# Kernel optimization log

Hardware: AMD Instinct MI355X
Metric: run time of the kernel (lower is better)

## Reference

```python
import jax, jax.numpy as jnp
import numpy as np

TOP_K = 2
NUM_EXPERTS = 64
TEMPERATURE = 1.0

def setup_inputs() -> dict:
    key = jax.random.key(0)
    ks = jax.random.split(key, 4)
    B, L, D, DT, E = 4, 4096, 2048, 16, NUM_EXPERTS
    return {
        "x": jax.random.normal(ks[0], (B, L, D), dtype=jnp.float32),
        "z_task": jax.random.normal(ks[1], (B, DT), dtype=jnp.float32),
        "W_router": jax.random.normal(ks[2], (E, D + DT), dtype=jnp.float32) * 0.02,
        "W_task_proj": jax.random.normal(ks[3], (DT, DT), dtype=jnp.float32) * 0.25,
        "b_task_proj": jnp.zeros((DT,), dtype=jnp.float32),
        "expert_bias": jnp.zeros((E,), dtype=jnp.float32),
    }

def reference(x, z_task, W_router, W_task_proj, b_task_proj, expert_bias):
    B, L, D = x.shape
    E = W_router.shape[0]
    DT = z_task.shape[-1]
    # task_proj: Linear(d_task, d_task) + exact GELU
    tp = jax.nn.gelu(z_task @ W_task_proj.T + b_task_proj, approximate=False)  # [B, DT]
    # concat fusion: logits = [x ; task_proj] @ W_router^T, split to avoid materializing concat
    logits = (jnp.einsum('bld,ed->ble', x, W_router[:, :D])
              + jnp.einsum('bt,et->be', tp, W_router[:, D:])[:, None, :]
              + expert_bias)  # [B, L, E]
    probs = jax.nn.softmax(logits / TEMPERATURE, axis=-1)
    topw, topi = jax.lax.top_k(probs, TOP_K)  # [B, L, K]
    topw = topw / (topw.sum(axis=-1, keepdims=True) + 1e-8)
    # aux load-balance loss: E * sum_i f_i * P_i over flattened tokens
    mask = jax.nn.one_hot(topi, E, dtype=probs.dtype).sum(axis=-2) / TOP_K  # [B, L, E]
    f = mask.reshape(-1, E).mean(axis=0)
    P = probs.reshape(-1, E).mean(axis=0)
    aux_loss = E * (f * P).sum()
    return topw, topi, probs, aux_loss
```

## Files before the change

kernel.cpp:

```cpp
#include <hip/hip_runtime.h>
#include <math.h>


#define DDIM 2048
#define WROW 2064

typedef unsigned int u32;
typedef unsigned short u16;
typedef unsigned long long u64;
using short8 = __attribute__((ext_vector_type(8))) short;
using f32x4  = __attribute__((ext_vector_type(4))) float;

typedef const __attribute__((address_space(1))) u32* gp1;
typedef __attribute__((address_space(3))) u32* lp3;

#define BAR() do {                                                              \
        __builtin_amdgcn_s_barrier();                                           \
        asm volatile("" ::: "memory");                                          \
        __builtin_amdgcn_sched_barrier(0);                                      \
    } while (0)

__device__ __forceinline__ u16 bf16rne(float f) {
    u32 u = __float_as_uint(f);
    return (u16)((u + 0x7FFFu + ((u >> 16) & 1u)) >> 16);
}

__global__ void k0_wsplit(const float* __restrict__ Wr, u32* __restrict__ wh,
                          u32* __restrict__ wl) {
    const int g = blockIdx.x * 256 + threadIdx.x;
    const int e  = g >> 10;
    const int kp = g & 1023;
    const int k  = kp * 2;
    const int step = k >> 5, kb = (k >> 3) & 3, d = (k >> 1) & 3;
    const int grp = e >> 4, lane = kb * 16 + (e & 15);
    const float w0 = Wr[(size_t)e * WROW + k];
    const float w1 = Wr[(size_t)e * WROW + k + 1];
    const u16 h0 = bf16rne(w0);
    const u16 h1 = bf16rne(w1);
    const u16 l0 = bf16rne(w0 - __uint_as_float((u32)h0 << 16));
    const u16 l1 = bf16rne(w1 - __uint_as_float((u32)h1 << 16));
    const u32 oi = (u32)(((step * 4 + grp) * 64 + lane) * 4 + d);
    wh[oi] = ((u32)h1 << 16) | h0;
    wl[oi] = ((u32)l1 << 16) | l0;
}

__global__ void k1_task(const float* __restrict__ z, const float* __restrict__ Wp,
                        const float* __restrict__ bp, const float* __restrict__ Wr,
                        const float* __restrict__ eb, float* __restrict__ wsb) {
    __shared__ float tp[4][16];
    const int t = threadIdx.x;
    if (t < 64) {
        const int b = t >> 4, r = t & 15;
        float s = bp[r];
        #pragma unroll
        for (int i = 0; i < 16; ++i) s += z[b * 16 + i] * Wp[r * 16 + i];
        tp[b][r] = 0.5f * s * (1.0f + erff(s * 0.70710678118654752440f));
    }
    #pragma unroll
    for (int i = t; i < 1024; i += 256) wsb[256 + i] = 0.0f;
    __syncthreads();
    {
        const int b = t >> 6, e = t & 63;
        const float* wr = Wr + (size_t)e * WROW + DDIM;
        float s = eb[e];
        #pragma unroll
        for (int i = 0; i < 16; ++i) s += tp[b][i] * wr[i];
        wsb[b * 64 + e] = s;
    }
}

__global__ __launch_bounds__(576, 1) void k2_mfma(const float* __restrict__ x,
                                                  const float* __restrict__ wsb,
                                                  const u32* __restrict__ whp,
                                                  const u32* __restrict__ wlp,
                                                  float* __restrict__ wacc,
                                                  float* __restrict__ out) {
    __shared__ __align__(16) u32  bbuf[2][4096];
    __shared__ float lg[2][64 * 68];
    __shared__ float pf[8 * 128];

    const int tid   = threadIdx.x;
    const int wv    = __builtin_amdgcn_readfirstlane(tid >> 6);
    const int lane  = tid & 63;
    const int tok0b = blockIdx.x * 64;
    const int bb    = tok0b >> 12;

    if (wv == 8) {
#define BDMA(t, buf) do {                                                       \
            _Pragma("unroll")                                                   \
            for (int hl = 0; hl < 2; ++hl)                                      \
            _Pragma("unroll")                                                   \
            for (int hh = 0; hh < 2; ++hh)                                      \
            _Pragma("unroll")                                                   \
            for (int g = 0; g < 4; ++g) {                                       \
                const u32* _s = (hl ? wlp : whp) +                              \
                                ((t) + hh * 32) * 1024 + g * 256 + lane * 4;    \
                u32* _d = &bbuf[buf][hl * 2048 + hh * 1024 + g * 256 + lane * 4];\
                __builtin_amdgcn_global_load_lds((gp1)_s, (lp3)_d, 16, 0, 0);   \
            }                                                                   \
        } while (0)
        BDMA(0, 0);
        asm volatile("s_waitcnt vmcnt(0)" ::: "memory");
        BAR();
        for (int t = 0; t < 32; ++t) {
            if (t < 31) {
                BDMA(t + 1, (t + 1) & 1);
                asm volatile("s_waitcnt vmcnt(0)" ::: "memory");
            }
            BAR();
        }
#undef BDMA
    } else {
        const int tg  = wv & 3;
        const int h   = wv >> 2;
        const int row = lane & 15;
        const int kg  = lane >> 4;
        const int tok0 = tok0b + tg * 16;

        f32x4 acc[4];
        #pragma unroll
        for (int g = 0; g < 4; ++g) {
            const float tl = (h == 0) ? wsb[bb * 64 + g * 16 + row] : 0.0f;
            acc[g] = (f32x4){tl, tl, tl, tl};
        }
        #pragma unroll
        for (int g = 0; g < 4; ++g) asm volatile("" : "+v"(acc[g]));
        __builtin_amdgcn_sched_barrier(0);

        const u64 xaddr = (u64)(x + (size_t)(tok0 + row) * DDIM + h * 1024 + kg * 8);
        f32x4 xr[6][2];

#define XLOAD(i, T) do {                                                        \
            asm volatile("global_load_dwordx4 %0, %1, off offset:%c2"           \
                : "=&v"(xr[i][0]) : "v"(xaddr), "i"((T) * 128));                \
            asm volatile("global_load_dwordx4 %0, %1, off offset:%c2"           \
                : "=&v"(xr[i][1]) : "v"(xaddr), "i"((T) * 128 + 16));           \
        } while (0)

#define XWAIT(i) do {                                                           \
            asm volatile("s_waitcnt vmcnt(10)"                                  \
                : "+v"(xr[i][0]), "+v"(xr[i][1]));                              \
            __builtin_amdgcn_sched_barrier(0);                                  \
        } while (0)

#define MSTEP(xa, xb, BH, BL) do {                                              \
            float vv[8];                                                        \
            _Pragma("unroll")                                                   \
            for (int j = 0; j < 4; ++j) { vv[j] = (xa)[j]; vv[4 + j] = (xb)[j]; }\
            short8 Ah, Al;                                                      \
            _Pragma("unroll")                                                   \
            for (int j = 0; j < 8; ++j) {                                       \
                const float v = vv[j];                                          \
                const u16 hh = bf16rne(v);                                      \
                const u16 ll = bf16rne(v - __uint_as_float((u32)hh << 16));     \
                Ah[j] = (short)hh; Al[j] = (short)ll;                           \
            }                                                                   \
            _Pragma("unroll")                                                   \
            for (int g = 0; g < 4; ++g) {                                       \
                acc[g] = __builtin_amdgcn_mfma_f32_16x16x32_bf16(Ah, BH[g], acc[g], 0, 0, 0); \
                acc[g] = __builtin_amdgcn_mfma_f32_16x16x32_bf16(Ah, BL[g], acc[g], 0, 0, 0); \
                acc[g] = __builtin_amdgcn_mfma_f32_16x16x32_bf16(Al, BH[g], acc[g], 0, 0, 0); \
                acc[g] = __builtin_amdgcn_mfma_f32_16x16x32_bf16(Al, BL[g], acc[g], 0, 0, 0); \
            }                                                                   \
        } while (0)

        XLOAD(0, 0); XLOAD(1, 1); XLOAD(2, 2);
        XLOAD(3, 3); XLOAD(4, 4); XLOAD(5, 5);
        BAR();
        #pragma unroll
        for (int t = 0; t < 32; ++t) {
            short8 BH[4], BL[4];
            #pragma unroll
            for (int g = 0; g < 4; ++g) {
                BH[g] = *(const short8*)&bbuf[t & 1][h * 1024 + g * 256 + lane * 4];
                BL[g] = *(const short8*)&bbuf[t & 1][2048 + h * 1024 + g * 256 + lane * 4];
            }
            XWAIT(t % 6);
            MSTEP(xr[t % 6][0], xr[t % 6][1], BH, BL);
            XLOAD(t % 6, (t + 6) & 31);
            BAR();
        }
        asm volatile("s_waitcnt vmcnt(0)"
            : "+v"(xr[0][0]), "+v"(xr[0][1]), "+v"(xr[1][0]), "+v"(xr[1][1]),
              "+v"(xr[2][0]), "+v"(xr[2][1]), "+v"(xr[3][0]), "+v"(xr[3][1]),
              "+v"(xr[4][0]), "+v"(xr[4][1]), "+v"(xr[5][0]), "+v"(xr[5][1]));
        __builtin_amdgcn_sched_barrier(0);
#undef XLOAD
#undef XWAIT
#undef MSTEP

        #pragma unroll
        for (int g = 0; g < 4; ++g)
            #pragma unroll
            for (int r = 0; r < 4; ++r)
                lg[h][(tg * 16 + kg * 4 + r) * 68 + g * 16 + row] = acc[g][r];
    }

    __syncthreads();

    if (wv < 8) {
        float pacc = 0.0f, facc = 0.0f;
        for (int i = 0; i < 8; ++i) {
            const int tk = wv * 8 + i;
            const float v = lg[0][tk * 68 + lane] + lg[1][tk * 68 + lane];
            float m1 = v; int i1 = lane;
            #pragma unroll
            for (int off = 32; off; off >>= 1) {
                const float ov = __shfl_xor(m1, off, 64);
                const int   oi = __shfl_xor(i1, off, 64);
                if (ov > m1 || (ov == m1 && oi < i1)) { m1 = ov; i1 = oi; }
            }
            const float vx = (lane == i1) ? -3.4e38f : v;
            float m2 = vx; int i2 = lane;
            #pragma unroll
            for (int off = 32; off; off >>= 1) {
                const float ov = __shfl_xor(m2, off, 64);
                const int   oi = __shfl_xor(i2, off, 64);
                if (ov > m2 || (ov == m2 && oi < i2)) { m2 = ov; i2 = oi; }
            }
            const float p = __expf(v - m1);
            float s = p;
            #pragma unroll
            for (int off = 32; off; off >>= 1) s += __shfl_xor(s, off, 64);
            const float rZ = 1.0f / s;
            const float pn = p * rZ;
            const int   T  = tok0b + tk;
            out[65536 + (size_t)T * 64 + lane] = pn;
            pacc += pn;
            facc += (lane == i1 ? 1.0f : 0.0f) + (lane == i2 ? 1.0f : 0.0f);
            if (lane == 0) {
                const float q1 = rZ, q2 = __expf(m2 - m1) * rZ;
                const float dn = 1.0f / (q1 + q2 + 1e-8f);
                float2 tw; tw.x = q1 * dn; tw.y = q2 * dn;
                *(float2*)(out + (size_t)T * 2) = tw;
                float2 ti; ti.x = (float)i1; ti.y = (float)i2;
                *(float2*)(out + 32768 + (size_t)T * 2) = ti;
            }
        }
        pf[wv * 128 + lane]      = pacc;
        pf[wv * 128 + 64 + lane] = facc;
    }
    __syncthreads();

    if (wv == 0) {
        float ps = 0.0f, fs = 0.0f;
        #pragma unroll
        for (int w2 = 0; w2 < 8; ++w2) {
            ps += pf[w2 * 128 + lane];
            fs += pf[w2 * 128 + 64 + lane];
        }
        const int slot = blockIdx.x & 7;
        atomicAdd(wacc + slot * 128 + lane, ps);
        atomicAdd(wacc + slot * 128 + 64 + lane, fs);
    }
}

__global__ void k3_aux(const float* __restrict__ wsb, float* __restrict__ out) {
    const int e = threadIdx.x;
    float P = 0.0f, F = 0.0f;
    #pragma unroll
    for (int s = 0; s < 8; ++s) {
        P += wsb[256 + s * 128 + e];
        F += wsb[256 + s * 128 + 64 + e];
    }
    float val = P * F;
    #pragma unroll
    for (int off = 32; off; off >>= 1) val += __shfl_xor(val, off, 64);
    if (e == 0)
        out[1114112] = 64.0f * val / (16384.0f * 2.0f * 16384.0f);
}

extern "C" void kernel_launch(void* const* d_in, const int* in_sizes, int n_in,
                              void* d_out, int out_size, void* d_ws, size_t ws_size,
                              hipStream_t stream) {
    (void)in_sizes; (void)n_in; (void)out_size; (void)ws_size;
    const float* x  = (const float*)d_in[0];
    const float* z  = (const float*)d_in[1];
    const float* Wr = (const float*)d_in[2];
    const float* Wp = (const float*)d_in[3];
    const float* bp = (const float*)d_in[4];
    const float* eb = (const float*)d_in[5];
    float* out = (float*)d_out;
    float* wsb = (float*)d_ws;
    u32*   wfH = (u32*)(wsb + 1280);
    u32*   wfL = wfH + 65536;

    hipLaunchKernelGGL(k0_wsplit, dim3(256), dim3(256), 0, stream, Wr, wfH, wfL);
    hipLaunchKernelGGL(k1_task,   dim3(1),   dim3(256), 0, stream, z, Wp, bp, Wr, eb, wsb);
    hipLaunchKernelGGL(k2_mfma,   dim3(256), dim3(576), 0, stream, x, wsb,
                       wfH, wfL, wsb + 256, out);
    hipLaunchKernelGGL(k3_aux,    dim3(1),   dim3(64),  0, stream, wsb, out);
}
```

Baseline: 55.90 us.

## Triple-buffer router weight DMA and alias LDS buffers into one pool

The producer wave now keeps two weight tiles in flight through a three-slot LDS ring, using a partial vmcnt wait instead of draining all loads before each barrier. The double-buffer, logits and partial-sum arrays are merged into one aliased shared pool so the extra slot adds no LDS. This is meant to hide global-to-LDS load latency behind the MFMA loop. Aliasing the logit scratch over the weight buffers depends on every DMA being finished before the epilogue writes to them, and the ring adds a modulo-3 index.

```diff
diff --git a/kernel.cpp b/kernel.cpp
--- a/kernel.cpp
+++ b/kernel.cpp
@@ -75,9 +75,9 @@
                                                   const u32* __restrict__ wlp,
                                                   float* __restrict__ wacc,
                                                   float* __restrict__ out) {
-    __shared__ __align__(16) u32  bbuf[2][4096];
-    __shared__ float lg[2][64 * 68];
-    __shared__ float pf[8 * 128];
+    __shared__ __align__(16) u32 smem[13312];
+    float* const lgf = (float*)smem;
+    float* const pff = (float*)&smem[12288];
 
     const int tid   = threadIdx.x;
     const int wv    = __builtin_amdgcn_readfirstlane(tid >> 6);
@@ -95,19 +95,19 @@
             for (int g = 0; g < 4; ++g) {                                       \
                 const u32* _s = (hl ? wlp : whp) +                              \
                                 ((t) + hh * 32) * 1024 + g * 256 + lane * 4;    \
-                u32* _d = &bbuf[buf][hl * 2048 + hh * 1024 + g * 256 + lane * 4];\
+                u32* _d = &smem[(buf) * 4096 + hl * 2048 + hh * 1024 + g * 256 + lane * 4];\
                 __builtin_amdgcn_global_load_lds((gp1)_s, (lp3)_d, 16, 0, 0);   \
             }                                                                   \
         } while (0)
         BDMA(0, 0);
         asm volatile("s_waitcnt vmcnt(0)" ::: "memory");
         BAR();
+        BDMA(1, 1); BDMA(2, 2);
         for (int t = 0; t < 32; ++t) {
-            if (t < 31) {
-                BDMA(t + 1, (t + 1) & 1);
-                asm volatile("s_waitcnt vmcnt(0)" ::: "memory");
-            }
+            if (t <= 29)      asm volatile("s_waitcnt vmcnt(16)" ::: "memory");
+            else if (t == 30) asm volatile("s_waitcnt vmcnt(0)"  ::: "memory");
             BAR();
+            if (t + 3 < 32) BDMA(t + 3, (t + 3) % 3);
         }
 #undef BDMA
     } else {
@@ -172,8 +172,8 @@
             short8 BH[4], BL[4];
             #pragma unroll
             for (int g = 0; g < 4; ++g) {
-                BH[g] = *(const short8*)&bbuf[t & 1][h * 1024 + g * 256 + lane * 4];
-                BL[g] = *(const short8*)&bbuf[t & 1][2048 + h * 1024 + g * 256 + lane * 4];
+                BH[g] = *(const short8*)&smem[(t % 3) * 4096 + h * 1024 + g * 256 + lane * 4];
+                BL[g] = *(const short8*)&smem[(t % 3) * 4096 + 2048 + h * 1024 + g * 256 + lane * 4];
             }
             XWAIT(t % 6);
             MSTEP(xr[t % 6][0], xr[t % 6][1], BH, BL);
@@ -193,7 +193,7 @@
         for (int g = 0; g < 4; ++g)
             #pragma unroll
             for (int r = 0; r < 4; ++r)
-                lg[h][(tg * 16 + kg * 4 + r) * 68 + g * 16 + row] = acc[g][r];
+                lgf[h * 4352 + (tg * 16 + kg * 4 + r) * 68 + g * 16 + row] = acc[g][r];
     }
 
     __syncthreads();
@@ -202,7 +202,7 @@
         float pacc = 0.0f, facc = 0.0f;
         for (int i = 0; i < 8; ++i) {
             const int tk = wv * 8 + i;
-            const float v = lg[0][tk * 68 + lane] + lg[1][tk * 68 + lane];
+            const float v = lgf[tk * 68 + lane] + lgf[4352 + tk * 68 + lane];
             float m1 = v; int i1 = lane;
             #pragma unroll
             for (int off = 32; off; off >>= 1) {
@@ -237,8 +237,8 @@
                 *(float2*)(out + 32768 + (size_t)T * 2) = ti;
             }
         }
-        pf[wv * 128 + lane]      = pacc;
-        pf[wv * 128 + 64 + lane] = facc;
+        pff[wv * 128 + lane]      = pacc;
+        pff[wv * 128 + 64 + lane] = facc;
     }
     __syncthreads();
 
@@ -246,8 +246,8 @@
         float ps = 0.0f, fs = 0.0f;
         #pragma unroll
         for (int w2 = 0; w2 < 8; ++w2) {
-            ps += pf[w2 * 128 + lane];
-            fs += pf[w2 * 128 + 64 + lane];
+            ps += pff[w2 * 128 + lane];
+            fs += pff[w2 * 128 + 64 + lane];
         }
         const int slot = blockIdx.x & 7;
         atomicAdd(wacc + slot * 128 + lane, ps);
```

Result: faster. 49.75 us (-11.0%).
